# Performance work log

Hardware: AMD Instinct MI355X
Metric: run time of the kernel (lower is better)

The kernel has to match this reference:

```python
import jax, jax.numpy as jnp
import numpy as np

SEQ, B, IN, H = 512, 64, 1024, 1024


def setup_inputs() -> dict:
    key = jax.random.key(0)
    k0, k1, k2, k3, k4 = jax.random.split(key, 5)
    stdv = 1.0 / np.sqrt(H)
    Xt = jax.random.normal(k0, (SEQ, B, IN), dtype=jnp.float32)
    # layer 0: concat(x[IN], h0[H]) -> H ; layer 1: concat(y0[H], h1[H]) -> H
    W0 = jax.random.uniform(k1, (H, IN + H), dtype=jnp.float32, minval=-stdv, maxval=stdv)
    b0 = jax.random.uniform(k2, (H,), dtype=jnp.float32, minval=-stdv, maxval=stdv)
    W1 = jax.random.uniform(k3, (H, H + H), dtype=jnp.float32, minval=-stdv, maxval=stdv)
    b1 = jax.random.uniform(k4, (H,), dtype=jnp.float32, minval=-stdv, maxval=stdv)
    return {"Xt": Xt, "W0": W0, "b0": b0, "W1": W1, "b1": b1}


def reference(Xt, W0, b0, W1, b1):
    # Concatenated-gate stacked tanh RNN (n_states=1), seq-major layout [S,B,F].
    Bsz = Xt.shape[1]
    h0 = jnp.zeros((Bsz, W0.shape[0]), dtype=Xt.dtype)
    h1 = jnp.zeros((Bsz, W1.shape[0]), dtype=Xt.dtype)

    def step(carry, x):
        h0, h1 = carry
        h0n = jnp.tanh(jnp.concatenate([x, h0], axis=-1) @ W0.T + b0)
        h1n = jnp.tanh(jnp.concatenate([h0n, h1], axis=-1) @ W1.T + b1)
        return (h0n, h1n), h1n

    (_, _), Y = jax.lax.scan(step, (h0, h1), Xt)
    return Y  # [SEQ, B, H] — stacked top-layer outputs (stack_output=True)
```

## Files before the change

kernel.cpp:

```cpp
#include <hip/hip_runtime.h>


typedef unsigned short ushort_t;
typedef unsigned int uint32;
typedef __attribute__((ext_vector_type(4))) unsigned int u32x4;
typedef __attribute__((ext_vector_type(4))) float f32x4;
typedef __attribute__((ext_vector_type(8))) __bf16 bfrag;

__device__ __forceinline__ f32x4 mfma_bf16(u32x4 a, u32x4 b, f32x4 c) {
  return __builtin_amdgcn_mfma_f32_16x16x32_bf16(
      __builtin_bit_cast(bfrag, a), __builtin_bit_cast(bfrag, b), c, 0, 0, 0);
}

__device__ __forceinline__ uint32 bf16rne(float f) {
  uint32 u = __builtin_bit_cast(uint32, f);
  return (u + 0x7fffu + ((u >> 16) & 1u)) >> 16;
}

__device__ __forceinline__ uint32 cvt_pk(float lo, float hi) {
  uint32 r;
  asm("v_cvt_pk_bf16_f32 %0, %1, %2" : "=v"(r) : "v"(lo), "v"(hi));
  return r;
}
__device__ __forceinline__ u32x4 pack8(f32x4 a, f32x4 b) {
  u32x4 r;
  r.x = cvt_pk(a.x, a.y);
  r.y = cvt_pk(a.z, a.w);
  r.z = cvt_pk(b.x, b.y);
  r.w = cvt_pk(b.z, b.w);
  return r;
}

template <int BOFF>
__device__ __forceinline__ void ld16(u32x4& d, const ushort_t* base) {
  asm volatile("global_load_dwordx4 %0, %1, off offset:%c2 sc0"
               : "=v"(d) : "v"(base), "i"(BOFF) : "memory");
}

#define LOADB(BUF, AP, KOFF)                 \
  ld16<(KOFF) * 2 + 0>(BUF[0], AP);          \
  ld16<(KOFF) * 2 + 64>(BUF[1], AP);         \
  ld16<(KOFF) * 2 + 128>(BUF[2], AP);        \
  ld16<(KOFF) * 2 + 192>(BUF[3], AP);        \
  ld16<(KOFF) * 2 + 256>(BUF[4], AP);        \
  ld16<(KOFF) * 2 + 320>(BUF[5], AP);        \
  ld16<(KOFF) * 2 + 384>(BUF[6], AP);        \
  ld16<(KOFF) * 2 + 448>(BUF[7], AP);

__global__ void rnn_init(int* c) {
  for (int k = threadIdx.x; k < 8193; k += 256) {
    int z = 0;
    asm volatile("global_store_dword %0, %1, off sc0 sc1"
                 :: "v"(c + k), "v"(z) : "memory");
  }
  asm volatile("s_waitcnt vmcnt(0)" ::: "memory");
}

__global__ __launch_bounds__(512) void rnn_main(
    const float* __restrict__ Xt, const float* __restrict__ W0,
    const float* __restrict__ b0, const float* __restrict__ W1,
    const float* __restrict__ b1, float* __restrict__ Y,
    ushort_t* hbuf, int* cnt) {
  __shared__ float part[2][4][16][17];
  __shared__ int s_slot;

  const int tid = threadIdx.x;
  const int wave = tid >> 6;
  const int lane = tid & 63;
  const int ln15 = lane & 15;
  const int lq = lane >> 4;
  const int n = wave & 3;
  const bool fin = wave < 4;

  uint32 xcc;
  asm("s_getreg_b32 %0, hwreg(HW_REG_XCC_ID)" : "=s"(xcc));
  const int xcd = xcc & 7;

  int* fbase  = cnt + xcd * 1024;
  int* abortp = cnt + 8192;

  if (tid == 0) {
    int one = 1, old;
    asm volatile("global_atomic_add %0, %1, %2, off sc0 sc1\n\ts_waitcnt vmcnt(0)"
                 : "=v"(old) : "v"(fbase), "v"(one) : "memory");
    s_slot = old & 31;
  }
  __syncthreads();
  const int slot = s_slot;
  const bool isL1 = slot >= 16;
  const int F0 = (slot & 15) * 64;
  const int fcol = F0 + n * 16 + ln15;
  const int row8 = ln15 & 7;

  const int* myf = (lane < 16) ? (fbase + 16 + ln15 * 16)
                  : (lane < 32) ? (fbase + 528 + ln15 * 16)
                                : (fbase + 16);
  int* myflag = fbase + (isL1 ? 528 : 16) + (slot & 15) * 16;

  const int kh = isL1 ? (fin ? 0 : 1) : (fin ? 1 : 0);
  const float* Wsrc = isL1 ? W1 : W0;

  u32x4 bw[32];
  {
    const float* wp = Wsrc + (size_t)fcol * 2048 + kh * 1024 + lq * 8;
#pragma unroll
    for (int j = 0; j < 32; ++j) {
      f32x4 w0 = *(const f32x4*)(wp + j * 32);
      f32x4 w1 = *(const f32x4*)(wp + j * 32 + 4);
      bw[j] = pack8(w0, w1);
    }
  }
  const float bia = fin ? (isL1 ? b1 : b0)[fcol] : 0.f;

  ushort_t* h0b = hbuf + (size_t)xcd * 40960;
  ushort_t* h1b = h0b + 24576;

  auto gemm_h = [&](const ushort_t* hsrc) -> f32x4 {
    f32x4 a = {0.f, 0.f, 0.f, 0.f};
    const ushort_t* ap = hsrc + row8 * 1024 + lq * 8;
    u32x4 fa[8], fb[8];
    LOADB(fa, ap, 0);
    LOADB(fb, ap, 256);
    asm volatile("s_waitcnt vmcnt(8)" ::: "memory");
    __builtin_amdgcn_sched_barrier(0);
#pragma unroll
    for (int j = 0; j < 8; ++j) a = mfma_bf16(fa[j], bw[j], a);
    LOADB(fa, ap, 512);
    asm volatile("s_waitcnt vmcnt(8)" ::: "memory");
    __builtin_amdgcn_sched_barrier(0);
#pragma unroll
    for (int j = 0; j < 8; ++j) a = mfma_bf16(fb[j], bw[8 + j], a);
    LOADB(fb, ap, 768);
    asm volatile("s_waitcnt vmcnt(8)" ::: "memory");
    __builtin_amdgcn_sched_barrier(0);
#pragma unroll
    for (int j = 0; j < 8; ++j) a = mfma_bf16(fa[j], bw[16 + j], a);
    asm volatile("s_waitcnt vmcnt(0)" ::: "memory");
    __builtin_amdgcn_sched_barrier(0);
#pragma unroll
    for (int j = 0; j < 8; ++j) a = mfma_bf16(fb[j], bw[24 + j], a);
    return a;
  };

  auto gemm_x = [&](int t) -> f32x4 {
    f32x4 a = {0.f, 0.f, 0.f, 0.f};
    const float* xp = Xt + ((size_t)t * 64 + xcd * 8 + row8) * 1024 + lq * 8;
#pragma unroll
    for (int j = 0; j < 32; ++j) {
      f32x4 x0 = *(const f32x4*)(xp + j * 32);
      f32x4 x1 = *(const f32x4*)(xp + j * 32 + 4);
      a = mfma_bf16(pack8(x0, x1), bw[j], a);
    }
    return a;
  };

  for (int t = 0; t < 512; ++t) {
    const int buf = t & 1;
    f32x4 acc = {0.f, 0.f, 0.f, 0.f};
    uint32 pf0 = 0, pf1 = 0;

    if (wave == 0) {
      const int tA = isL1 ? t + 1 : t;
      const int tB = isL1 ? t : t - 2;
      const int tgt = (lane < 16) ? tA : (lane < 32) ? tB : -2000000000;
      if (tA > 0) {
        for (int it = 0;; ++it) {
          int v;
          asm volatile("global_load_dword %0, %1, off sc0 sc1\n\ts_waitcnt vmcnt(0)"
                       : "=v"(v) : "v"(myf) : "memory");
          if (__all(v >= tgt)) break;
          asm volatile("s_sleep 2" ::: "memory");
          if ((it & 255) == 255) {
            int a;
            asm volatile("global_load_dword %0, %1, off sc0 sc1\n\ts_waitcnt vmcnt(0)"
                         : "=v"(a) : "v"(abortp) : "memory");
            if (a) break;
            if (it > (1 << 18)) {
              int one = 1;
              asm volatile("global_store_dword %0, %1, off sc0 sc1\n\ts_waitcnt vmcnt(0)"
                           :: "v"(abortp), "v"(one) : "memory");
              break;
            }
          }
        }
      }
    } else if (!isL1 && !fin) {
      {
        int tn = t < 511 ? t + 1 : 511;
        const char* pfp = (const char*)(Xt + ((size_t)tn * 64 + xcd * 8) * 1024)
                          + n * 8192 + lane * 128;
        asm volatile("global_load_dword %0, %1, off" : "=v"(pf0) : "v"(pfp));
        asm volatile("global_load_dword %0, %1, off offset:64" : "=v"(pf1) : "v"(pfp));
      }
      acc = gemm_x(t);
#pragma unroll
      for (int r = 0; r < 4; ++r) part[buf][n][lq * 4 + r][ln15] = acc[r];
    }
    __syncthreads();

    if (!isL1) {
      if (fin && t >= 1) acc = gemm_h(h0b + ((t - 1) % 3) * 8192);
    } else {
      if (fin) {
        acc = gemm_h(h0b + (t % 3) * 8192);
      } else {
        if (t >= 1) acc = gemm_h(h1b + ((t - 1) & 1) * 8192);
#pragma unroll
        for (int r = 0; r < 4; ++r) part[buf][n][lq * 4 + r][ln15] = acc[r];
      }
    }
    if (!fin) asm volatile("" :: "v"(pf0), "v"(pf1));
    __syncthreads();

    if (fin) {
      float o[4];
#pragma unroll
      for (int r = 0; r < 4; ++r) {
        float s = acc[r] + part[buf][n][lq * 4 + r][ln15] + bia;
        float ax = fabsf(s);
        float e = __expf(2.f * ax);
        float rr = 1.f - 2.f * __builtin_amdgcn_rcpf(e + 1.f);
        o[r] = copysignf(rr, s);
      }
      if (lq < 2) {
        ushort_t* hd = (isL1 ? h1b + (t & 1) * 8192 : h0b + (t % 3) * 8192)
                       + (lq * 4) * 1024 + fcol;
#pragma unroll
        for (int r = 0; r < 4; ++r) {
          uint32 hv = bf16rne(o[r]);
          asm volatile("global_store_short %0, %1, off sc0"
                       :: "v"(hd + r * 1024), "v"(hv) : "memory");
        }
        if (isL1) {
          float* yd = Y + ((size_t)t * 64 + xcd * 8 + lq * 4) * 1024 + fcol;
#pragma unroll
          for (int r = 0; r < 4; ++r) yd[r * 1024] = o[r];
        }
      }
      asm volatile("s_waitcnt vmcnt(0)" ::: "memory");
    }
    __syncthreads();

    if (tid == 0) {
      int val = t + 1;
      asm volatile("global_store_dword %0, %1, off sc0 sc1"
                   :: "v"(myflag), "v"(val) : "memory");
    }
  }
}

extern "C" void kernel_launch(void* const* d_in, const int* in_sizes, int n_in,
                              void* d_out, int out_size, void* d_ws, size_t ws_size,
                              hipStream_t stream) {
  const float* Xt = (const float*)d_in[0];
  const float* W0 = (const float*)d_in[1];
  const float* b0 = (const float*)d_in[2];
  const float* W1 = (const float*)d_in[3];
  const float* b1 = (const float*)d_in[4];
  float* Y = (float*)d_out;

  int* cnt = (int*)d_ws;
  ushort_t* hbuf = (ushort_t*)((char*)d_ws + 36864);

  rnn_init<<<1, 256, 0, stream>>>(cnt);
  rnn_main<<<256, 512, 0, stream>>>(Xt, W0, b0, W1, b1, Y, hbuf, cnt);
}
```

Before: 6.311 ms.

## Add fast packed-flag polling via scalar loads with fallback to slow per-slot flags

Adds a second set of progress flags, 16 consecutive ints per layer within a single cache line per XCD. Workgroups poll them with scalar loads after an s_dcache_inv and take the minimum across the line, instead of issuing vector loads to flags spread across separate lines. If the fast path does not see progress within a bounded number of iterations, the block falls back permanently to the original sc0/sc1 polling. This is meant to cut inter-workgroup synchronization latency per timestep, at the cost of extra flag stores and reliance on coherence behaviour that is only established within an XCD.

```diff
diff --git a/kernel.cpp b/kernel.cpp
--- a/kernel.cpp
+++ b/kernel.cpp
@@ -3,6 +3,7 @@
 
 typedef unsigned short ushort_t;
 typedef unsigned int uint32;
+typedef __attribute__((ext_vector_type(4))) int i32x4;
 typedef __attribute__((ext_vector_type(4))) unsigned int u32x4;
 typedef __attribute__((ext_vector_type(4))) float f32x4;
 typedef __attribute__((ext_vector_type(8))) __bf16 bfrag;
@@ -47,6 +48,24 @@
   ld16<(KOFF) * 2 + 384>(BUF[6], AP);        \
   ld16<(KOFF) * 2 + 448>(BUF[7], AP);
 
+__device__ __forceinline__ int line_min16(const int* p, int doInv) {
+  i32x4 q0, q1, q2, q3;
+  if (doInv) asm volatile("s_dcache_inv" ::: "memory");
+  asm volatile(
+      "s_load_dwordx4 %0, %4, 0x0\n\t"
+      "s_load_dwordx4 %1, %4, 0x10\n\t"
+      "s_load_dwordx4 %2, %4, 0x20\n\t"
+      "s_load_dwordx4 %3, %4, 0x30\n\t"
+      "s_waitcnt lgkmcnt(0)"
+      : "=s"(q0), "=s"(q1), "=s"(q2), "=s"(q3)
+      : "s"(p) : "memory");
+  int m = min(min(q0.x, q0.y), min(q0.z, q0.w));
+  m = min(m, min(min(q1.x, q1.y), min(q1.z, q1.w)));
+  m = min(m, min(min(q2.x, q2.y), min(q2.z, q2.w)));
+  m = min(m, min(min(q3.x, q3.y), min(q3.z, q3.w)));
+  return m;
+}
+
 __global__ void rnn_init(int* c) {
   for (int k = threadIdx.x; k < 8193; k += 256) {
     int z = 0;
@@ -92,10 +111,20 @@
   const int fcol = F0 + n * 16 + ln15;
   const int row8 = ln15 & 7;
 
+  const int* fl0p = fbase + 896;
+  const int* fl1p = fbase + 912;
+  int* fastflag = fbase + (isL1 ? 912 : 896) + (slot & 15);
+
   const int* myf = (lane < 16) ? (fbase + 16 + ln15 * 16)
                   : (lane < 32) ? (fbase + 528 + ln15 * 16)
                                 : (fbase + 16);
-  int* myflag = fbase + (isL1 ? 528 : 16) + (slot & 15) * 16;
+  int* slowflag = fbase + (isL1 ? 528 : 16) + (slot & 15) * 16;
+
+  if ((slot & 15) == 0 && tid < 16) {
+    int z = 0;
+    asm volatile("global_store_dword %0, %1, off sc0"
+                 :: "v"((int*)(fbase + (isL1 ? 912 : 896) + tid)), "v"(z) : "memory");
+  }
 
   const int kh = isL1 ? (fin ? 0 : 1) : (fin ? 1 : 0);
   const float* Wsrc = isL1 ? W1 : W0;
@@ -154,6 +183,8 @@
     return a;
   };
 
+  int mode = 0;
+
   for (int t = 0; t < 512; ++t) {
     const int buf = t & 1;
     f32x4 acc = {0.f, 0.f, 0.f, 0.f};
@@ -162,8 +193,25 @@
     if (wave == 0) {
       const int tA = isL1 ? t + 1 : t;
       const int tB = isL1 ? t : t - 2;
-      const int tgt = (lane < 16) ? tA : (lane < 32) ? tB : -2000000000;
-      if (tA > 0) {
+      const bool needA = tA >= 1, needB = tB >= 1;
+      const bool eligA = needA && tA >= 2 && !mode;
+      const bool eligB = needB && tB >= 2 && !mode;
+      bool fastDone = false;
+      if (eligA || eligB) {
+        for (int it = 0; it < 512; ++it) {
+          int mA = line_min16(fl0p, 1);
+          int mB = line_min16(fl1p, 0);
+          if ((!eligA || mA >= tA) && (!eligB || mB >= tB)) { fastDone = true; break; }
+          asm volatile("s_sleep 1" ::: "memory");
+        }
+        if (!fastDone) mode = 1;
+      }
+      const bool llcA = needA && (!eligA || !fastDone);
+      const bool llcB = needB && (!eligB || !fastDone);
+      if (llcA || llcB) {
+        const int tgt = (lane < 16) ? (llcA ? tA : (int)0x80000000)
+                       : (lane < 32) ? (llcB ? tB : (int)0x80000000)
+                                     : (int)0x80000000;
         for (int it = 0;; ++it) {
           int v;
           asm volatile("global_load_dword %0, %1, off sc0 sc1\n\ts_waitcnt vmcnt(0)"
@@ -243,8 +291,11 @@
 
     if (tid == 0) {
       int val = t + 1;
+      if (t >= 1)
+        asm volatile("global_store_dword %0, %1, off sc0"
+                     :: "v"(fastflag), "v"(val) : "memory");
       asm volatile("global_store_dword %0, %1, off sc0 sc1"
-                   :: "v"(myflag), "v"(val) : "memory");
+                   :: "v"(slowflag), "v"(val) : "memory");
     }
   }
 }
```

After: 6.076 ms. -3.7%, faster.
